# Kernel tuning notes

Hardware: AMD Instinct MI355X
Metric: run time of the kernel (lower is better)

The kernel has to match this reference:

```python
import jax, jax.numpy as jnp
import numpy as np

D_MODEL = 256
B, H, T = 4, 8, 2048
EPS = 1e-8


def _clinear(x_r, x_i, w_r, w_i, b_r, b_i):
    # complex matmul: (x_r + i x_i) @ (w_r + i w_i)^T + (b_r + i b_i)
    y_r = jnp.matmul(x_r, w_r.T) - jnp.matmul(x_i, w_i.T) + b_r
    y_i = jnp.matmul(x_i, w_r.T) + jnp.matmul(x_r, w_i.T) + b_i
    return y_r, y_i


def setup_inputs() -> dict:
    key = jax.random.key(0)
    ks = jax.random.split(key, 24)
    d = D_MODEL
    std = np.sqrt(2.0 / (d + d)) / np.sqrt(2.0)  # glorot-ish * 1/sqrt(2) as in _init_weights
    inp = {}
    inp['q_in_r'] = jax.random.normal(ks[0], (B, H, T, d), jnp.float32)
    inp['q_in_i'] = jax.random.normal(ks[1], (B, H, T, d), jnp.float32)
    inp['kv_in_r'] = jax.random.normal(ks[2], (B, H, T, d), jnp.float32)
    inp['kv_in_i'] = jax.random.normal(ks[3], (B, H, T, d), jnp.float32)
    i = 4
    for p in ['q', 'k', 'v', 'o']:
        inp[p + '_wr'] = std * jax.random.normal(ks[i], (d, d), jnp.float32); i += 1
        inp[p + '_wi'] = std * jax.random.normal(ks[i], (d, d), jnp.float32); i += 1
        inp[p + '_br'] = jnp.zeros((d,), jnp.float32)
        inp[p + '_bi'] = jnp.zeros((d,), jnp.float32)
    inp['gate_w'] = std * jax.random.normal(ks[i], (d, d), jnp.float32)
    inp['gate_b'] = jnp.zeros((d,), jnp.float32)
    return inp


def reference(q_in_r, q_in_i, kv_in_r, kv_in_i,
              q_wr, q_wi, q_br, q_bi,
              k_wr, k_wi, k_br, k_bi,
              v_wr, v_wi, v_br, v_bi,
              o_wr, o_wi, o_br, o_bi,
              gate_w, gate_b):
    D = q_in_r.shape[-1]
    q_r, q_i = _clinear(q_in_r, q_in_i, q_wr, q_wi, q_br, q_bi)
    k_r, k_i = _clinear(kv_in_r, kv_in_i, k_wr, k_wi, k_br, k_bi)
    v_r, v_i = _clinear(kv_in_r, kv_in_i, v_wr, v_wi, v_br, v_bi)
    scale = 1.0 / np.sqrt(D)
    # real part of complex inner product <q, k> (the module's dual-part score)
    scores = (jnp.einsum('bhqd,bhkd->bhqk', q_r, k_r)
              + jnp.einsum('bhqd,bhkd->bhqk', q_i, k_i)) * scale
    attn = jax.nn.softmax(scores, axis=-1)
    ctx_r = jnp.einsum('bhqk,bhkd->bhqd', attn, v_r)
    ctx_i = jnp.einsum('bhqk,bhkd->bhqd', attn, v_i)
    out_r, out_i = _clinear(ctx_r, ctx_i, o_wr, o_wi, o_br, o_bi)
    out_mag = jnp.sqrt(out_r ** 2 + out_i ** 2 + EPS)
    gate = jax.nn.sigmoid(jnp.matmul(out_mag, gate_w.T) + gate_b)
    return out_r * gate, out_i * gate
```

## Files before the change

kernel.cpp:

```cpp
#include <hip/hip_runtime.h>
#include <hip/hip_bf16.h>
#include <hip/hip_fp16.h>
#include <stdint.h>


#define TSEQ   2048
#define NHEADS 32
#define MTOT   65536
#define DDC    512
#define HCHUNK 8

typedef float    f32x4  __attribute__((ext_vector_type(4)));
typedef _Float16 f16x8  __attribute__((ext_vector_type(8)));
typedef uint16_t u16x4  __attribute__((ext_vector_type(4)));
typedef uint16_t u16x8  __attribute__((ext_vector_type(8)));

__device__ __forceinline__ uint16_t f2h(float f) {
  _Float16 h = (_Float16)f;
  return __builtin_bit_cast(uint16_t, h);
}
__device__ __forceinline__ float h2f(uint16_t u) {
  return (float)__builtin_bit_cast(_Float16, u);
}

__device__ __forceinline__ void gld16(const void* g, void* l) {
  __builtin_amdgcn_global_load_lds(
      (const __attribute__((address_space(1))) uint32_t*)g,
      (__attribute__((address_space(3))) uint32_t*)l, 16, 0, 0);
}

enum { EP_F16Z = 0, EP_PROJ = 1, EP_OUT = 2, EP_GATE = 3 };

template <int EP>
__global__ __launch_bounds__(256, 2) void gemm_bt(
    const uint16_t* __restrict__ A, int lda, long zA,
    const uint16_t* __restrict__ B, int ldb, long zB,
    void* __restrict__ C, int ldc, long zC, int K,
    const float* __restrict__ biasR, const float* __restrict__ biasI,
    float scale, float* __restrict__ outR, float* __restrict__ outI) {
  __shared__ uint16_t lds[2 * 128 * 32];
  uint16_t* lA = lds;
  uint16_t* lB = lds + 128 * 32;
  const int tid  = threadIdx.x;
  const int wave = tid >> 6;
  const int lane = tid & 63;
  const int wr   = (wave >> 1) * 64;
  const int wc   = (wave & 1) * 64;

  const int gx = gridDim.x, gy = gridDim.y;
  const int nwg = gx * gy * gridDim.z;
  const int lin = blockIdx.x + gx * (blockIdx.y + gy * blockIdx.z);
  const int cpx = nwg >> 3;
  const int swz = (lin & 7) * cpx + (lin >> 3);
  const int shx = __popc(gx - 1);
  const int shy = __popc(gy - 1);
  const int bx = swz & (gx - 1);
  const int by = (swz >> shx) & (gy - 1);
  const int bz = swz >> (shx + shy);

  const long tm  = (long)by * 128;
  const long tn  = (long)bx * 128;
  const uint16_t* Ab = A + (long)bz * zA;
  const uint16_t* Bb = B + (long)bz * zB;

  f32x4 acc[4][4] = {};

  const int  srow  = wave * 16 + (lane >> 2);
  const int  skoff = (lane & 3) * 8;
  uint16_t* lA0 = lA + (wave * 16) * 32;
  uint16_t* lA1 = lA + (64 + wave * 16) * 32;
  uint16_t* lB0 = lB + (wave * 16) * 32;
  uint16_t* lB1 = lB + (64 + wave * 16) * 32;

  const int fr = lane & 15;
  const int fk = (lane >> 4) * 8;

  const int nK = K >> 5;
  for (int kb = 0; kb < nK; ++kb) {
    const long k0 = (long)kb * 32 + skoff;
    __syncthreads();
    gld16(Ab + (tm + srow) * (long)lda + k0,      lA0);
    gld16(Ab + (tm + 64 + srow) * (long)lda + k0, lA1);
    gld16(Bb + (tn + srow) * (long)ldb + k0,      lB0);
    gld16(Bb + (tn + 64 + srow) * (long)ldb + k0, lB1);
    __syncthreads();

    f16x8 af[4], bf[4];
#pragma unroll
    for (int i = 0; i < 4; ++i)
      af[i] = *(const f16x8*)&lA[(wr + i * 16 + fr) * 32 + fk];
#pragma unroll
    for (int j = 0; j < 4; ++j)
      bf[j] = *(const f16x8*)&lB[(wc + j * 16 + fr) * 32 + fk];
#pragma unroll
    for (int i = 0; i < 4; ++i)
#pragma unroll
      for (int j = 0; j < 4; ++j)
        acc[i][j] = __builtin_amdgcn_mfma_f32_16x16x32_f16(af[i], bf[j], acc[i][j], 0, 0, 0);
  }

  const int quad = lane >> 4;

  if constexpr (EP == EP_F16Z || EP == EP_PROJ) {
    __syncthreads();
    char* wreg = (char*)(lds + wave * 2048);
    uint16_t* Cp = (uint16_t*)C + ((EP == EP_F16Z) ? (long)bz * zC : 0L);
#pragma unroll
    for (int p = 0; p < 2; ++p) {
#pragma unroll
      for (int jl = 0; jl < 2; ++jl) {
        const int j = p * 2 + jl;
#pragma unroll
        for (int i = 0; i < 4; ++i) {
#pragma unroll
          for (int r = 0; r < 4; ++r) {
            const int row  = i * 16 + quad * 4 + r;
            const int colv = jl * 16 + fr;
            int byte = row * 64 + colv * 2;
            byte ^= ((row >> 2) & 3) << 5;
            float v = acc[i][j][r];
            if constexpr (EP == EP_PROJ) {
              const int col = (int)tn + wc + p * 32 + colv;
              v += (col < 256) ? biasR[col] : biasI[col - 256];
            } else {
              v *= scale;
            }
            *(uint16_t*)(wreg + byte) = f2h(v);
          }
        }
      }
      asm volatile("s_waitcnt lgkmcnt(0)" ::: "memory");
      __builtin_amdgcn_sched_barrier(0);
#pragma unroll
      for (int t4 = 0; t4 < 4; ++t4) {
        const int row = t4 * 16 + (lane >> 2);
        const int c   = lane & 3;
        int byte = row * 64 + c * 16;
        byte ^= ((row >> 2) & 3) << 5;
        const u16x8 val = *(const u16x8*)(wreg + byte);
        const long grow = tm + wr + row;
        const int  gcol = (int)tn + wc + p * 32 + c * 8;
        *(u16x8*)(Cp + grow * (long)ldc + gcol) = val;
      }
      if (p == 0) {
        asm volatile("s_waitcnt lgkmcnt(0)" ::: "memory");
        __builtin_amdgcn_sched_barrier(0);
      }
    }
  } else {
#pragma unroll
    for (int i = 0; i < 4; ++i) {
      const long row0 = tm + wr + i * 16 + quad * 4;
#pragma unroll
      for (int j = 0; j < 4; ++j) {
        const int col = (int)tn + wc + j * 16 + fr;
#pragma unroll
        for (int r = 0; r < 4; ++r) {
          float v = acc[i][j][r];
          const long rw = row0 + r;
          if constexpr (EP == EP_OUT) {
            if (col < 256) outR[rw * 256 + col]       = v + biasR[col];
            else           outI[rw * 256 + col - 256] = v + biasI[col - 256];
          } else {
            const float g = 1.0f / (1.0f + __expf(-(v + biasR[col])));
            const long o = rw * 256 + col;
            outR[o] *= g;
            outI[o] *= g;
          }
        }
      }
    }
  }
}

__global__ void pack_x(const float* __restrict__ xr, const float* __restrict__ xi,
                       uint16_t* __restrict__ out) {
  const long idx = (long)blockIdx.x * 256 + threadIdx.x;
  const long m  = idx >> 7;
  const int  c4 = (int)(idx & 127) << 2;
  const float* src = (c4 < 256) ? (xr + m * 256 + c4) : (xi + m * 256 + (c4 - 256));
  const float4 v = *(const float4*)src;
  u16x4 o = {f2h(v.x), f2h(v.y), f2h(v.z), f2h(v.w)};
  *(u16x4*)(out + m * 512 + c4) = o;
}

__global__ void pack_w(const float* __restrict__ wr, const float* __restrict__ wi,
                       uint16_t* __restrict__ out) {
  const int idx = blockIdx.x * 256 + threadIdx.x;
  const int j  = idx >> 7;
  const int c4 = (idx & 127) << 2;
  const float* src;
  float sgn = 1.f;
  if (j < 256) {
    if (c4 < 256) src = wr + j * 256 + c4;
    else { src = wi + j * 256 + (c4 - 256); sgn = -1.f; }
  } else {
    if (c4 < 256) src = wi + (j - 256) * 256 + c4;
    else          src = wr + (j - 256) * 256 + (c4 - 256);
  }
  const float4 v = *(const float4*)src;
  u16x4 o = {f2h(sgn * v.x), f2h(sgn * v.y), f2h(sgn * v.z), f2h(sgn * v.w)};
  *(u16x4*)(out + (long)j * 512 + c4) = o;
}

__global__ void pack_gw(const float* __restrict__ w, uint16_t* __restrict__ out) {
  const int idx = blockIdx.x * 256 + threadIdx.x;
  const float4 v = *(const float4*)(w + (long)idx * 4);
  u16x4 o = {f2h(v.x), f2h(v.y), f2h(v.z), f2h(v.w)};
  *(u16x4*)(out + (long)idx * 4) = o;
}

__global__ void transpose_v(const uint16_t* __restrict__ V, uint16_t* __restrict__ Vt) {
  __shared__ uint16_t t[32][33];
  const int h = blockIdx.z;
  const uint16_t* Vh = V + (long)h * TSEQ * DDC;
  uint16_t* Vth = Vt + (long)h * DDC * TSEQ;
  const int t0 = blockIdx.x * 32;
  const int n0 = blockIdx.y * 32;
  const int lx = threadIdx.x & 31, ly = threadIdx.x >> 5;
#pragma unroll
  for (int yy = ly; yy < 32; yy += 8)
    t[yy][lx] = Vh[(long)(t0 + yy) * DDC + n0 + lx];
  __syncthreads();
#pragma unroll
  for (int yy = ly; yy < 32; yy += 8)
    Vth[(long)(n0 + yy) * TSEQ + t0 + lx] = t[lx][yy];
}

__global__ __launch_bounds__(256) void softmax_rows(uint16_t* __restrict__ S) {
  const long row = blockIdx.x;
  uint16_t* p = S + row * 2048;
  const int tid = threadIdx.x;
  u16x8 raw = ((const u16x8*)p)[tid];
  float v[8];
#pragma unroll
  for (int j = 0; j < 8; ++j) v[j] = h2f(raw[j]);
  float m = v[0];
#pragma unroll
  for (int j = 1; j < 8; ++j) m = fmaxf(m, v[j]);
#pragma unroll
  for (int off = 32; off >= 1; off >>= 1) m = fmaxf(m, __shfl_xor(m, off));
  __shared__ float red[8];
  const int wave = tid >> 6, lane = tid & 63;
  if (lane == 0) red[wave] = m;
  __syncthreads();
  m = fmaxf(fmaxf(red[0], red[1]), fmaxf(red[2], red[3]));
  float s = 0.f;
#pragma unroll
  for (int j = 0; j < 8; ++j) { v[j] = __expf(v[j] - m); s += v[j]; }
#pragma unroll
  for (int off = 32; off >= 1; off >>= 1) s += __shfl_xor(s, off);
  if (lane == 0) red[4 + wave] = s;
  __syncthreads();
  s = red[4] + red[5] + red[6] + red[7];
  const float inv = 1.0f / s;
  u16x8 o;
#pragma unroll
  for (int j = 0; j < 8; ++j) o[j] = f2h(v[j] * inv);
  ((u16x8*)p)[tid] = o;
}

__global__ void mag_kernel(const float* __restrict__ R, const float* __restrict__ I,
                           uint16_t* __restrict__ mag) {
  const long i = ((long)blockIdx.x * 256 + threadIdx.x) * 4;
  const float4 r  = *(const float4*)(R + i);
  const float4 im = *(const float4*)(I + i);
  u16x4 o = {f2h(sqrtf(r.x * r.x + im.x * im.x + 1e-8f)),
             f2h(sqrtf(r.y * r.y + im.y * im.y + 1e-8f)),
             f2h(sqrtf(r.z * r.z + im.z * im.z + 1e-8f)),
             f2h(sqrtf(r.w * r.w + im.w * im.w + 1e-8f))};
  *(u16x4*)(mag + i) = o;
}

extern "C" void kernel_launch(void* const* d_in, const int* in_sizes, int n_in,
                              void* d_out, int out_size, void* d_ws, size_t ws_size,
                              hipStream_t stream) {
  const float* q_in_r  = (const float*)d_in[0];
  const float* q_in_i  = (const float*)d_in[1];
  const float* kv_in_r = (const float*)d_in[2];
  const float* kv_in_i = (const float*)d_in[3];
  const float* q_wr = (const float*)d_in[4];
  const float* q_wi = (const float*)d_in[5];
  const float* q_br = (const float*)d_in[6];
  const float* q_bi = (const float*)d_in[7];
  const float* k_wr = (const float*)d_in[8];
  const float* k_wi = (const float*)d_in[9];
  const float* k_br = (const float*)d_in[10];
  const float* k_bi = (const float*)d_in[11];
  const float* v_wr = (const float*)d_in[12];
  const float* v_wi = (const float*)d_in[13];
  const float* v_br = (const float*)d_in[14];
  const float* v_bi = (const float*)d_in[15];
  const float* o_wr = (const float*)d_in[16];
  const float* o_wi = (const float*)d_in[17];
  const float* o_br = (const float*)d_in[18];
  const float* o_bi = (const float*)d_in[19];
  const float* gate_w = (const float*)d_in[20];
  const float* gate_b = (const float*)d_in[21];

  unsigned char* w = (unsigned char*)d_ws;
  const size_t MAT16 = (size_t)MTOT * DDC * 2;
  size_t off = 0;
  uint16_t* R1 = (uint16_t*)(w + off); off += MAT16;
  uint16_t* R2 = (uint16_t*)(w + off); off += MAT16;
  uint16_t* R3 = (uint16_t*)(w + off); off += MAT16;
  uint16_t* R4 = (uint16_t*)(w + off); off += MAT16;
  uint16_t* R5 = (uint16_t*)(w + off); off += MAT16;
  uint16_t* Wq = (uint16_t*)(w + off); off += 512 * 512 * 2;
  uint16_t* Wk = (uint16_t*)(w + off); off += 512 * 512 * 2;
  uint16_t* Wv = (uint16_t*)(w + off); off += 512 * 512 * 2;
  uint16_t* Wo = (uint16_t*)(w + off); off += 512 * 512 * 2;
  uint16_t* Gw = (uint16_t*)(w + off); off += 256 * 256 * 2;

  uint16_t* Xq  = R1; uint16_t* Vt  = R1;
  uint16_t* Xkv = R2; uint16_t* Ctx = R2;
  uint16_t* Qm  = R3; uint16_t* Mag = R3;
  uint16_t* Km  = R4;
  uint16_t* Vm  = R5; uint16_t* Sc  = R5;

  float* outR = (float*)d_out;
  float* outI = (float*)d_out + (long)MTOT * 256;

  pack_x<<<32768, 256, 0, stream>>>(q_in_r, q_in_i, Xq);
  pack_x<<<32768, 256, 0, stream>>>(kv_in_r, kv_in_i, Xkv);
  pack_w<<<256, 256, 0, stream>>>(q_wr, q_wi, Wq);
  pack_w<<<256, 256, 0, stream>>>(k_wr, k_wi, Wk);
  pack_w<<<256, 256, 0, stream>>>(v_wr, v_wi, Wv);
  pack_w<<<256, 256, 0, stream>>>(o_wr, o_wi, Wo);
  pack_gw<<<64, 256, 0, stream>>>(gate_w, Gw);

  gemm_bt<EP_PROJ><<<dim3(4, 512, 1), 256, 0, stream>>>(
      Xq, 512, 0, Wq, 512, 0, Qm, 512, 0, 512, q_br, q_bi, 1.f, nullptr, nullptr);
  gemm_bt<EP_PROJ><<<dim3(4, 512, 1), 256, 0, stream>>>(
      Xkv, 512, 0, Wk, 512, 0, Km, 512, 0, 512, k_br, k_bi, 1.f, nullptr, nullptr);
  gemm_bt<EP_PROJ><<<dim3(4, 512, 1), 256, 0, stream>>>(
      Xkv, 512, 0, Wv, 512, 0, Vm, 512, 0, 512, v_br, v_bi, 1.f, nullptr, nullptr);
  transpose_v<<<dim3(64, 16, 32), 256, 0, stream>>>(Vm, Vt);

  for (int c = 0; c < NHEADS / HCHUNK; ++c) {
    const long ho = (long)c * HCHUNK;
    gemm_bt<EP_F16Z><<<dim3(16, 16, HCHUNK), 256, 0, stream>>>(
        Qm + ho * TSEQ * DDC, 512, (long)TSEQ * DDC,
        Km + ho * TSEQ * DDC, 512, (long)TSEQ * DDC,
        Sc, TSEQ, (long)TSEQ * TSEQ, 512, nullptr, nullptr, 0.0625f, nullptr, nullptr);
    softmax_rows<<<HCHUNK * TSEQ, 256, 0, stream>>>(Sc);
    gemm_bt<EP_F16Z><<<dim3(4, 16, HCHUNK), 256, 0, stream>>>(
        Sc, TSEQ, (long)TSEQ * TSEQ,
        Vt + ho * DDC * TSEQ, TSEQ, (long)DDC * TSEQ,
        Ctx + ho * TSEQ * DDC, 512, (long)TSEQ * DDC, 2048,
        nullptr, nullptr, 1.f, nullptr, nullptr);
  }

  gemm_bt<EP_OUT><<<dim3(4, 512, 1), 256, 0, stream>>>(
      Ctx, 512, 0, Wo, 512, 0, nullptr, 0, 0, 512, o_br, o_bi, 1.f, outR, outI);

  mag_kernel<<<16384, 256, 0, stream>>>(outR, outI, Mag);

  gemm_bt<EP_GATE><<<dim3(2, 512, 1), 256, 0, stream>>>(
      Mag, 256, 0, Gw, 256, 0, nullptr, 0, 0, 256, gate_b, nullptr, 1.f, outR, outI);
}
```

Measured before the change: 1.248 ms.

## Enlarge GEMM tiles to 256x256 with 8 waves, double-buffered BK=64 LDS pipeline

Reworks the generic GEMM kernel to use 512-thread workgroups with BMx256 output tiles (BM 256 or 128), K-step 64, XOR-swizzled LDS layout, and double-buffered async global-to-LDS staging that overlaps the next tile's loads with the current MFMA work. Larger tiles raise arithmetic intensity and cut global traffic per FLOP, and the prefetch removes the load-then-sync stall of the previous single-buffer loop. The cost is a much larger LDS footprint (up to 128 KB per block for BM=256) and more accumulator registers, which may reduce occupancy, and fewer workgroups for the smaller GEMMs.

New measurement: 1.137 ms. 8.9% less time.

```diff
diff --git a/kernel.cpp b/kernel.cpp
--- a/kernel.cpp
+++ b/kernel.cpp
@@ -31,21 +31,24 @@
 
 enum { EP_F16Z = 0, EP_PROJ = 1, EP_OUT = 2, EP_GATE = 3 };
 
-template <int EP>
-__global__ __launch_bounds__(256, 2) void gemm_bt(
+template <int EP, int BM>
+__global__ __launch_bounds__(512, 2) void gemm_bt(
     const uint16_t* __restrict__ A, int lda, long zA,
     const uint16_t* __restrict__ B, int ldb, long zB,
     void* __restrict__ C, int ldc, long zC, int K,
     const float* __restrict__ biasR, const float* __restrict__ biasI,
     float scale, float* __restrict__ outR, float* __restrict__ outI) {
-  __shared__ uint16_t lds[2 * 128 * 32];
-  uint16_t* lA = lds;
-  uint16_t* lB = lds + 128 * 32;
+  constexpr int MI    = BM / 32;
+  constexpr int ASLAB = BM / 64;
+  constexpr int ABUFE = BM * 64;
+  constexpr int BUFE  = (BM + 256) * 64;
+  __shared__ uint16_t lds[2 * BUFE];
+
   const int tid  = threadIdx.x;
   const int wave = tid >> 6;
   const int lane = tid & 63;
-  const int wr   = (wave >> 1) * 64;
-  const int wc   = (wave & 1) * 64;
+  const int wr   = (wave >> 2) * (BM / 2);
+  const int wc   = (wave & 3) * 64;
 
   const int gx = gridDim.x, gy = gridDim.y;
   const int nwg = gx * gy * gridDim.z;
@@ -58,98 +61,108 @@
   const int by = (swz >> shx) & (gy - 1);
   const int bz = swz >> (shx + shy);
 
-  const long tm  = (long)by * 128;
-  const long tn  = (long)bx * 128;
+  const long tm = (long)by * BM;
+  const long tn = (long)bx * 256;
   const uint16_t* Ab = A + (long)bz * zA;
   const uint16_t* Bb = B + (long)bz * zB;
 
-  f32x4 acc[4][4] = {};
-
-  const int  srow  = wave * 16 + (lane >> 2);
-  const int  skoff = (lane & 3) * 8;
-  uint16_t* lA0 = lA + (wave * 16) * 32;
-  uint16_t* lA1 = lA + (64 + wave * 16) * 32;
-  uint16_t* lB0 = lB + (wave * 16) * 32;
-  uint16_t* lB1 = lB + (64 + wave * 16) * 32;
-
-  const int fr = lane & 15;
-  const int fk = (lane >> 4) * 8;
-
-  const int nK = K >> 5;
-  for (int kb = 0; kb < nK; ++kb) {
-    const long k0 = (long)kb * 32 + skoff;
+  f32x4 acc[MI][4] = {};
+
+  const int arow   = wave * 8 + (lane >> 3);
+  const int schunk = (lane & 7) ^ (lane >> 3);
+
+  const int fr   = lane & 15;
+  const int quad = lane >> 4;
+  const int sw   = fr & 7;
+  const int ch0  = ((0 + quad) ^ sw) * 16;
+  const int ch1  = ((4 + quad) ^ sw) * 16;
+
+  const int nt = K >> 6;
+
+  auto STAGE = [&](int buf, int t) {
+    const long k0 = (long)t * 64 + schunk * 8;
+    uint16_t* base = lds + buf * BUFE;
+#pragma unroll
+    for (int s = 0; s < ASLAB; ++s)
+      gld16(Ab + (tm + s * 64 + arow) * (long)lda + k0,
+            base + (s * 64 + wave * 8) * 64);
+#pragma unroll
+    for (int s = 0; s < 4; ++s)
+      gld16(Bb + (tn + s * 64 + arow) * (long)ldb + k0,
+            base + ABUFE + (s * 64 + wave * 8) * 64);
+  };
+
+  auto COMPUTE = [&](int buf) {
+    const char* Abase = (const char*)(lds + buf * BUFE);
+    const char* Bbase = Abase + 2 * ABUFE;
+#pragma unroll
+    for (int ks = 0; ks < 2; ++ks) {
+      const int co = ks ? ch1 : ch0;
+      f16x8 bf[4];
+#pragma unroll
+      for (int j = 0; j < 4; ++j)
+        bf[j] = *(const f16x8*)(Bbase + (wc + j * 16 + fr) * 128 + co);
+#pragma unroll
+      for (int i = 0; i < MI; ++i) {
+        const f16x8 af = *(const f16x8*)(Abase + (wr + i * 16 + fr) * 128 + co);
+#pragma unroll
+        for (int j = 0; j < 4; ++j)
+          acc[i][j] = __builtin_amdgcn_mfma_f32_16x16x32_f16(af, bf[j], acc[i][j], 0, 0, 0);
+      }
+    }
+  };
+
+  STAGE(0, 0);
+  __syncthreads();
+  int cur = 0;
+  for (int t = 0; t + 1 < nt; ++t) {
+    STAGE(cur ^ 1, t + 1);
+    COMPUTE(cur);
     __syncthreads();
-    gld16(Ab + (tm + srow) * (long)lda + k0,      lA0);
-    gld16(Ab + (tm + 64 + srow) * (long)lda + k0, lA1);
-    gld16(Bb + (tn + srow) * (long)ldb + k0,      lB0);
-    gld16(Bb + (tn + 64 + srow) * (long)ldb + k0, lB1);
-    __syncthreads();
-
-    f16x8 af[4], bf[4];
-#pragma unroll
-    for (int i = 0; i < 4; ++i)
-      af[i] = *(const f16x8*)&lA[(wr + i * 16 + fr) * 32 + fk];
-#pragma unroll
-    for (int j = 0; j < 4; ++j)
-      bf[j] = *(const f16x8*)&lB[(wc + j * 16 + fr) * 32 + fk];
-#pragma unroll
-    for (int i = 0; i < 4; ++i)
-#pragma unroll
-      for (int j = 0; j < 4; ++j)
-        acc[i][j] = __builtin_amdgcn_mfma_f32_16x16x32_f16(af[i], bf[j], acc[i][j], 0, 0, 0);
+    cur ^= 1;
   }
-
-  const int quad = lane >> 4;
+  COMPUTE(cur);
 
   if constexpr (EP == EP_F16Z || EP == EP_PROJ) {
     __syncthreads();
-    char* wreg = (char*)(lds + wave * 2048);
+    char* wbase = (char*)lds + wave * (BM * 64);
     uint16_t* Cp = (uint16_t*)C + ((EP == EP_F16Z) ? (long)bz * zC : 0L);
 #pragma unroll
-    for (int p = 0; p < 2; ++p) {
-#pragma unroll
-      for (int jl = 0; jl < 2; ++jl) {
-        const int j = p * 2 + jl;
-#pragma unroll
-        for (int i = 0; i < 4; ++i) {
-#pragma unroll
-          for (int r = 0; r < 4; ++r) {
-            const int row  = i * 16 + quad * 4 + r;
-            const int colv = jl * 16 + fr;
-            int byte = row * 64 + colv * 2;
-            byte ^= ((row >> 2) & 3) << 5;
-            float v = acc[i][j][r];
-            if constexpr (EP == EP_PROJ) {
-              const int col = (int)tn + wc + p * 32 + colv;
-              v += (col < 256) ? biasR[col] : biasI[col - 256];
-            } else {
-              v *= scale;
-            }
-            *(uint16_t*)(wreg + byte) = f2h(v);
+    for (int i = 0; i < MI; ++i) {
+#pragma unroll
+      for (int j = 0; j < 4; ++j) {
+#pragma unroll
+        for (int r = 0; r < 4; ++r) {
+          const int row = i * 16 + quad * 4 + r;
+          int byte = row * 128 + (j * 16 + fr) * 2;
+          byte ^= ((row >> 2) & 3) << 5;
+          float v = acc[i][j][r];
+          if constexpr (EP == EP_PROJ) {
+            const int col = (int)tn + wc + j * 16 + fr;
+            v += (col < 256) ? biasR[col] : biasI[col - 256];
+          } else {
+            v *= scale;
           }
+          *(uint16_t*)(wbase + byte) = f2h(v);
         }
       }
-      asm volatile("s_waitcnt lgkmcnt(0)" ::: "memory");
-      __builtin_amdgcn_sched_barrier(0);
-#pragma unroll
-      for (int t4 = 0; t4 < 4; ++t4) {
-        const int row = t4 * 16 + (lane >> 2);
-        const int c   = lane & 3;
-        int byte = row * 64 + c * 16;
-        byte ^= ((row >> 2) & 3) << 5;
-        const u16x8 val = *(const u16x8*)(wreg + byte);
-        const long grow = tm + wr + row;
-        const int  gcol = (int)tn + wc + p * 32 + c * 8;
-        *(u16x8*)(Cp + grow * (long)ldc + gcol) = val;
-      }
-      if (p == 0) {
-        asm volatile("s_waitcnt lgkmcnt(0)" ::: "memory");
-        __builtin_amdgcn_sched_barrier(0);
-      }
+    }
+    asm volatile("s_waitcnt lgkmcnt(0)" ::: "memory");
+    __builtin_amdgcn_sched_barrier(0);
+#pragma unroll
+    for (int it = 0; it < BM / 16; ++it) {
+      const int row = it * 8 + (lane >> 3);
+      const int c   = lane & 7;
+      int byte = row * 128 + c * 16;
+      byte ^= ((row >> 2) & 3) << 5;
+      const u16x8 val = *(const u16x8*)(wbase + byte);
+      const long grow = tm + wr + row;
+      const int  gcol = (int)tn + wc + c * 8;
+      *(u16x8*)(Cp + grow * (long)ldc + gcol) = val;
     }
   } else {
 #pragma unroll
-    for (int i = 0; i < 4; ++i) {
+    for (int i = 0; i < MI; ++i) {
       const long row0 = tm + wr + i * 16 + quad * 4;
 #pragma unroll
       for (int j = 0; j < 4; ++j) {
@@ -329,33 +342,33 @@
   pack_w<<<256, 256, 0, stream>>>(o_wr, o_wi, Wo);
   pack_gw<<<64, 256, 0, stream>>>(gate_w, Gw);
 
-  gemm_bt<EP_PROJ><<<dim3(4, 512, 1), 256, 0, stream>>>(
+  gemm_bt<EP_PROJ, 256><<<dim3(2, 256, 1), 512, 0, stream>>>(
       Xq, 512, 0, Wq, 512, 0, Qm, 512, 0, 512, q_br, q_bi, 1.f, nullptr, nullptr);
-  gemm_bt<EP_PROJ><<<dim3(4, 512, 1), 256, 0, stream>>>(
+  gemm_bt<EP_PROJ, 256><<<dim3(2, 256, 1), 512, 0, stream>>>(
       Xkv, 512, 0, Wk, 512, 0, Km, 512, 0, 512, k_br, k_bi, 1.f, nullptr, nullptr);
-  gemm_bt<EP_PROJ><<<dim3(4, 512, 1), 256, 0, stream>>>(
+  gemm_bt<EP_PROJ, 256><<<dim3(2, 256, 1), 512, 0, stream>>>(
       Xkv, 512, 0, Wv, 512, 0, Vm, 512, 0, 512, v_br, v_bi, 1.f, nullptr, nullptr);
   transpose_v<<<dim3(64, 16, 32), 256, 0, stream>>>(Vm, Vt);
 
   for (int c = 0; c < NHEADS / HCHUNK; ++c) {
     const long ho = (long)c * HCHUNK;
-    gemm_bt<EP_F16Z><<<dim3(16, 16, HCHUNK), 256, 0, stream>>>(
+    gemm_bt<EP_F16Z, 256><<<dim3(8, 8, HCHUNK), 512, 0, stream>>>(
         Qm + ho * TSEQ * DDC, 512, (long)TSEQ * DDC,
         Km + ho * TSEQ * DDC, 512, (long)TSEQ * DDC,
         Sc, TSEQ, (long)TSEQ * TSEQ, 512, nullptr, nullptr, 0.0625f, nullptr, nullptr);
     softmax_rows<<<HCHUNK * TSEQ, 256, 0, stream>>>(Sc);
-    gemm_bt<EP_F16Z><<<dim3(4, 16, HCHUNK), 256, 0, stream>>>(
+    gemm_bt<EP_F16Z, 128><<<dim3(2, 16, HCHUNK), 512, 0, stream>>>(
         Sc, TSEQ, (long)TSEQ * TSEQ,
         Vt + ho * DDC * TSEQ, TSEQ, (long)DDC * TSEQ,
         Ctx + ho * TSEQ * DDC, 512, (long)TSEQ * DDC, 2048,
         nullptr, nullptr, 1.f, nullptr, nullptr);
   }
 
-  gemm_bt<EP_OUT><<<dim3(4, 512, 1), 256, 0, stream>>>(
+  gemm_bt<EP_OUT, 256><<<dim3(2, 256, 1), 512, 0, stream>>>(
       Ctx, 512, 0, Wo, 512, 0, nullptr, 0, 0, 512, o_br, o_bi, 1.f, outR, outI);
 
   mag_kernel<<<16384, 256, 0, stream>>>(outR, outI, Mag);
 
-  gemm_bt<EP_GATE><<<dim3(2, 512, 1), 256, 0, stream>>>(
+  gemm_bt<EP_GATE, 256><<<dim3(1, 256, 1), 512, 0, stream>>>(
       Mag, 256, 0, Gw, 256, 0, nullptr, 0, 0, 256, gate_b, nullptr, 1.f, outR, outI);
 }
```
